# Performance work log

Hardware: AMD Instinct MI355X
Metric: run time of the kernel (lower is better)

The kernel has to match this reference:

```python
import jax, jax.numpy as jnp
import numpy as np

IN_CH = 128
OUT_CH = 32
HEADS = 4
N_NODES = 50000
N_EDGES = 500000
NEG_SLOPE = 0.01  # torch leaky_relu default


def setup_inputs() -> dict:
    key = jax.random.key(0)
    ks = jax.random.split(key, 8)
    E, D, H, C = N_EDGES, IN_CH, HEADS, OUT_CH
    receivers = jax.random.normal(ks[0], (E, D), dtype=jnp.float32)
    senders = jax.random.normal(ks[1], (E, D), dtype=jnp.float32)
    edge_attribute = jax.random.normal(ks[2], (E, D), dtype=jnp.float32)
    sender_idx = jax.random.randint(ks[3], (E,), 0, N_NODES)
    receiver_idx = jax.random.randint(ks[4], (E,), 0, N_NODES)
    # bias-free linear weights, stored as [in, heads*out] so y = x @ W
    scale = 1.0 / np.sqrt(D)
    W_src = jax.random.normal(ks[5], (D, H * C), dtype=jnp.float32) * scale
    W_tgt = jax.random.normal(ks[6], (D, H * C), dtype=jnp.float32) * scale
    W_edge = jax.random.normal(ks[7], (D, H * C), dtype=jnp.float32) * scale
    # xavier_normal_ on shape (1, H, C): std = sqrt(2/(H + C)) per torch fan calc on last two dims
    attn = jax.random.normal(jax.random.fold_in(key, 99), (1, H, C), dtype=jnp.float32) * np.sqrt(2.0 / (H + C))
    return {
        "receivers": receivers,
        "senders": senders,
        "edge_attribute": edge_attribute,
        "sender_idx": sender_idx,
        "receiver_idx": receiver_idx,
        "W_src": W_src,
        "W_tgt": W_tgt,
        "W_edge": W_edge,
        "attn": attn,
    }


def reference(receivers, senders, edge_attribute, sender_idx, receiver_idx, W_src, W_tgt, W_edge, attn):
    E = receivers.shape[0]
    H, C = HEADS, OUT_CH
    t = (receivers @ W_tgt).reshape(E, H, C)   # target projection of receiver feats
    s = (senders @ W_src).reshape(E, H, C)
    e = (edge_attribute @ W_edge).reshape(E, H, C)
    z = (jax.nn.leaky_relu(s + t + e, NEG_SLOPE) * attn).sum(-1)  # [E, H]
    # segment softmax over edges grouped by sender_idx
    zmax = jax.ops.segment_max(z, sender_idx, num_segments=N_NODES)  # [N, H]
    ez = jnp.exp(z - zmax[sender_idx])
    denom = jax.ops.segment_sum(ez, sender_idx, num_segments=N_NODES)
    a = ez / denom[sender_idx]                 # [E, H]
    m = t * a[..., None]                        # [E, H, C]
    aggr_m = jax.ops.segment_sum(m, receiver_idx, num_segments=N_NODES)  # [N, H, C]
    return aggr_m.mean(axis=1), m.mean(axis=1)  # ([N, C], [E, C])
```

## Files before the change

### kernel.cpp

```cpp
#include <hip/hip_runtime.h>
#include <hip/hip_bf16.h>

#define E_EDGES 500000
#define NN 50000

typedef unsigned short u16;
typedef __attribute__((ext_vector_type(8))) short s16x8;
typedef __attribute__((ext_vector_type(4))) float f32x4;

#define BAR() __builtin_amdgcn_s_barrier()
#define SCHED0() __builtin_amdgcn_sched_barrier(0)
#define WAITLGKM0() asm volatile("s_waitcnt lgkmcnt(0)" ::: "memory")

__device__ __forceinline__ short f2bf(float f) {
    unsigned u = __builtin_bit_cast(unsigned, f);
    u += 0x7fffu + ((u >> 16) & 1u);
    return (short)(u >> 16);
}

__device__ __forceinline__ float lrelu(float x) { return x > 0.0f ? x : 0.01f * x; }

__device__ __forceinline__ s16x8 cvt8(float4 lo, float4 hi) {
    union { s16x8 v; __hip_bfloat162 h[4]; } u;
    u.h[0] = __float22bfloat162_rn(make_float2(lo.x, lo.y));
    u.h[1] = __float22bfloat162_rn(make_float2(lo.z, lo.w));
    u.h[2] = __float22bfloat162_rn(make_float2(hi.x, hi.y));
    u.h[3] = __float22bfloat162_rn(make_float2(hi.z, hi.w));
    return u.v;
}

__global__ void kprep(const float* __restrict__ Wsrc, const float* __restrict__ Wtgt,
                      const float* __restrict__ Wedge, u16* __restrict__ WT) {
    int i = blockIdx.x * 256 + threadIdx.x;
    if (i >= 3 * 16384) return;
    int g = i >> 14, nk = i & 16383, n = nk >> 7, k = nk & 127;
    const float* W = (g == 0) ? Wsrc : (g == 1) ? Wtgt : Wedge;
    WT[i] = (u16)f2bf(W[k * 128 + n]);
}

__global__ __launch_bounds__(256, 2) void k1(
    const float* __restrict__ recv, const float* __restrict__ send,
    const float* __restrict__ eattr, const int* __restrict__ sidx,
    const u16* __restrict__ WT, const float* __restrict__ attn,
    float* __restrict__ ez, float* __restrict__ denom)
{
    __shared__ u16 ldsA[64][136];
    __shared__ u16 ldsB[128][136];
    __shared__ float smEz[64][4];
    const int tid = threadIdx.x;
    const int lane = tid & 63, wv = tid >> 6;
    const int l15 = lane & 15, lg = (lane >> 4) & 3;
    const int wm = wv >> 1, wn = wv & 1;
    const int row0 = blockIdx.x * 64;

    const float* Xg[3] = {send, eattr, recv};
    const int bgoff[3] = {0, 2 * 16384, 1 * 16384};

    f32x4 acc[2][4];
#pragma unroll
    for (int m = 0; m < 2; ++m)
#pragma unroll
        for (int ni = 0; ni < 4; ++ni) acc[m][ni] = (f32x4){0.f, 0.f, 0.f, 0.f};

    float4 ra[4][2];

    auto issueA = [&](int g) {
        const float* X = Xg[g];
#pragma unroll
        for (int q = 0; q < 4; ++q) {
            int idx = tid + 256 * q;
            int row = idx >> 4, gcol = (idx & 15) * 8;
            int ge = min(row0 + row, E_EDGES - 1);
            const float* p = X + (size_t)ge * 128 + gcol;
            ra[q][0] = *(const float4*)p;
            ra[q][1] = *(const float4*)(p + 4);
        }
    };

    auto commitA = [&]() {
#pragma unroll
        for (int q = 0; q < 4; ++q) {
            int idx = tid + 256 * q;
            *(s16x8*)&ldsA[idx >> 4][(idx & 15) * 8] = cvt8(ra[q][0], ra[q][1]);
        }
    };

    auto mfma_g = [&]() {
#pragma unroll
        for (int kk = 0; kk < 4; ++kk) {
            int k0 = kk * 32 + lg * 8;
            s16x8 a0 = *(const s16x8*)&ldsA[wm * 32 + l15][k0];
            s16x8 a1 = *(const s16x8*)&ldsA[wm * 32 + 16 + l15][k0];
#pragma unroll
            for (int ni = 0; ni < 4; ++ni) {
                s16x8 b = *(const s16x8*)&ldsB[(wn * 4 + ni) * 16 + l15][k0];
                acc[0][ni] = __builtin_amdgcn_mfma_f32_16x16x32_bf16(a0, b, acc[0][ni], 0, 0, 0);
                acc[1][ni] = __builtin_amdgcn_mfma_f32_16x16x32_bf16(a1, b, acc[1][ni], 0, 0, 0);
            }
        }
    };

    issueA(0);
#pragma unroll
    for (int g = 0; g < 3; ++g) {
        if (g) { mfma_g(); SCHED0(); }
        BAR();
        s16x8 rb[8];
        {
            const u16* Bg = WT + bgoff[g];
#pragma unroll
            for (int q = 0; q < 8; ++q) {
                int idx = tid + 256 * q;
                rb[q] = *(const s16x8*)(Bg + (idx >> 4) * 128 + (idx & 15) * 8);
            }
        }
        commitA();
        if (g < 2) issueA(g + 1);
        SCHED0();
#pragma unroll
        for (int q = 0; q < 8; ++q) {
            int idx = tid + 256 * q;
            *(s16x8*)&ldsB[idx >> 4][(idx & 15) * 8] = rb[q];
        }
        SCHED0();
        WAITLGKM0();
        BAR();
    }
    mfma_g();

    float av[4];
#pragma unroll
    for (int ni = 0; ni < 4; ++ni) av[ni] = attn[(wn * 4 + ni) * 16 + l15];

#pragma unroll
    for (int m = 0; m < 2; ++m) {
#pragma unroll
        for (int hh = 0; hh < 2; ++hh) {
            float part[4];
#pragma unroll
            for (int j = 0; j < 4; ++j)
                part[j] = lrelu(acc[m][2 * hh][j]) * av[2 * hh] +
                          lrelu(acc[m][2 * hh + 1][j]) * av[2 * hh + 1];
#pragma unroll
            for (int off = 1; off < 16; off <<= 1) {
#pragma unroll
                for (int j = 0; j < 4; ++j) part[j] += __shfl_xor(part[j], off, 64);
            }
            if (l15 == hh) {
#pragma unroll
                for (int j = 0; j < 4; ++j)
                    smEz[wm * 32 + m * 16 + lg * 4 + j][2 * wn + hh] = __expf(part[j]);
            }
        }
    }
    __syncthreads();
    {
        int row = tid >> 2, h = tid & 3;
        int r = row0 + row;
        float v = smEz[row][h];
        if (r < E_EDGES) {
            ez[(size_t)r * 4 + h] = v;
            int s = sidx[r];
            atomicAdd(&denom[(size_t)s * 4 + h], v);
        }
    }
}

__global__ __launch_bounds__(256, 2) void k2(
    const float* __restrict__ recv, const int* __restrict__ ridx,
    const int* __restrict__ sidx, const u16* __restrict__ WTt,
    const float* __restrict__ ez, const float* __restrict__ denom,
    float* __restrict__ out0, float* __restrict__ out1)
{
    __shared__ u16 ldsA[64][136];
    __shared__ u16 ldsB[128][136];
    const int tid = threadIdx.x;
    const int lane = tid & 63, wv = tid >> 6;
    const int l15 = lane & 15, lg = (lane >> 4) & 3;
    const int row0 = blockIdx.x * 64;

    float4 ra[4][2];
#pragma unroll
    for (int q = 0; q < 4; ++q) {
        int idx = tid + 256 * q;
        int row = idx >> 4, gcol = (idx & 15) * 8;
        int ge = min(row0 + row, E_EDGES - 1);
        const float* p = recv + (size_t)ge * 128 + gcol;
        ra[q][0] = *(const float4*)p;
        ra[q][1] = *(const float4*)(p + 4);
    }
    s16x8 rb[8];
#pragma unroll
    for (int q = 0; q < 8; ++q) {
        int idx = tid + 256 * q;
        rb[q] = *(const s16x8*)(WTt + (idx >> 4) * 128 + (idx & 15) * 8);
    }
#pragma unroll
    for (int q = 0; q < 4; ++q) {
        int idx = tid + 256 * q;
        *(s16x8*)&ldsA[idx >> 4][(idx & 15) * 8] = cvt8(ra[q][0], ra[q][1]);
    }
#pragma unroll
    for (int q = 0; q < 8; ++q) {
        int idx = tid + 256 * q;
        *(s16x8*)&ldsB[idx >> 4][(idx & 15) * 8] = rb[q];
    }
    __syncthreads();

    f32x4 acc[8];
#pragma unroll
    for (int n = 0; n < 8; ++n) acc[n] = (f32x4){0.f, 0.f, 0.f, 0.f};

#pragma unroll
    for (int kk = 0; kk < 4; ++kk) {
        int k0 = kk * 32 + lg * 8;
        s16x8 a = *(const s16x8*)&ldsA[wv * 16 + l15][k0];
#pragma unroll
        for (int n = 0; n < 8; ++n) {
            s16x8 b = *(const s16x8*)&ldsB[n * 16 + l15][k0];
            acc[n] = __builtin_amdgcn_mfma_f32_16x16x32_bf16(a, b, acc[n], 0, 0, 0);
        }
    }

#pragma unroll
    for (int j = 0; j < 4; ++j) {
        int r = row0 + wv * 16 + lg * 4 + j;
        if (r < E_EDGES) {
            int s = sidx[r];
            float4 ezv = *(const float4*)(ez + (size_t)r * 4);
            float4 dn = *(const float4*)(denom + (size_t)s * 4);
            float a0 = ezv.x / dn.x, a1 = ezv.y / dn.y;
            float a2 = ezv.z / dn.z, a3 = ezv.w / dn.w;
            float lo = 0.25f * (acc[0][j] * a0 + acc[2][j] * a1 +
                                acc[4][j] * a2 + acc[6][j] * a3);
            float hi = 0.25f * (acc[1][j] * a0 + acc[3][j] * a1 +
                                acc[5][j] * a2 + acc[7][j] * a3);
            out1[(size_t)r * 32 + l15] = lo;
            out1[(size_t)r * 32 + 16 + l15] = hi;
            int rv = ridx[r];
            atomicAdd(&out0[(size_t)rv * 32 + l15], lo);
            atomicAdd(&out0[(size_t)rv * 32 + 16 + l15], hi);
        }
    }
}

extern "C" void kernel_launch(void* const* d_in, const int* in_sizes, int n_in,
                              void* d_out, int out_size, void* d_ws, size_t ws_size,
                              hipStream_t stream) {
    const float* recv  = (const float*)d_in[0];
    const float* send  = (const float*)d_in[1];
    const float* eattr = (const float*)d_in[2];
    const int*   sidx  = (const int*)d_in[3];
    const int*   ridx  = (const int*)d_in[4];
    const float* Wsrc  = (const float*)d_in[5];
    const float* Wtgt  = (const float*)d_in[6];
    const float* Wedge = (const float*)d_in[7];
    const float* attn  = (const float*)d_in[8];

    char* ws = (char*)d_ws;
    u16*   WT    = (u16*)ws;
    float* ez    = (float*)(ws + 131072);
    float* denom = (float*)(ws + 131072 + 8000000);

    float* out0 = (float*)d_out;
    float* out1 = out0 + (size_t)NN * 32;

    hipMemsetAsync(denom, 0, (size_t)NN * 4 * sizeof(float), stream);
    hipMemsetAsync(out0, 0, (size_t)NN * 32 * sizeof(float), stream);

    kprep<<<192, 256, 0, stream>>>(Wsrc, Wtgt, Wedge, WT);

    int nb = (E_EDGES + 63) / 64;
    k1<<<nb, 256, 0, stream>>>(recv, send, eattr, sidx, WT, attn, ez, denom);
    k2<<<nb, 256, 0, stream>>>(recv, ridx, sidx, WT + 16384, ez, denom, out0, out1);
}
```

Measured before the change: 283.6 us.

## Make k1 persistent with register-resident weight fragments and per-wave head ownership

```diff
diff --git a/kernel.cpp b/kernel.cpp
--- a/kernel.cpp
+++ b/kernel.cpp
@@ -45,32 +45,37 @@
     float* __restrict__ ez, float* __restrict__ denom)
 {
     __shared__ u16 ldsA[64][136];
-    __shared__ u16 ldsB[128][136];
     __shared__ float smEz[64][4];
     const int tid = threadIdx.x;
     const int lane = tid & 63, wv = tid >> 6;
     const int l15 = lane & 15, lg = (lane >> 4) & 3;
-    const int wm = wv >> 1, wn = wv & 1;
-    const int row0 = blockIdx.x * 64;
+    const int b = blockIdx.x;
 
     const float* Xg[3] = {send, eattr, recv};
     const int bgoff[3] = {0, 2 * 16384, 1 * 16384};
 
-    f32x4 acc[2][4];
-#pragma unroll
-    for (int m = 0; m < 2; ++m)
-#pragma unroll
-        for (int ni = 0; ni < 4; ++ni) acc[m][ni] = (f32x4){0.f, 0.f, 0.f, 0.f};
-
+    s16x8 bfr[3][4][2];
+#pragma unroll
+    for (int g = 0; g < 3; ++g)
+#pragma unroll
+        for (int kk = 0; kk < 4; ++kk)
+#pragma unroll
+            for (int nn = 0; nn < 2; ++nn)
+                bfr[g][kk][nn] = *(const s16x8*)(WT + bgoff[g] +
+                    ((wv * 2 + nn) * 16 + l15) * 128 + kk * 32 + lg * 8);
+
+    const float av0 = attn[(wv * 2 + 0) * 16 + l15];
+    const float av1 = attn[(wv * 2 + 1) * 16 + l15];
+
+    f32x4 acc[4][2];
     float4 ra[4][2];
 
-    auto issueA = [&](int g) {
-        const float* X = Xg[g];
+    auto issueA = [&](const float* X, int tileRow) {
 #pragma unroll
         for (int q = 0; q < 4; ++q) {
             int idx = tid + 256 * q;
             int row = idx >> 4, gcol = (idx & 15) * 8;
-            int ge = min(row0 + row, E_EDGES - 1);
+            int ge = min(tileRow + row, E_EDGES - 1);
             const float* p = X + (size_t)ge * 128 + gcol;
             ra[q][0] = *(const float4*)p;
             ra[q][1] = *(const float4*)(p + 4);
@@ -85,83 +90,72 @@
         }
     };
 
-    auto mfma_g = [&]() {
+    auto mfma_ph = [&](const s16x8 (&bf)[4][2]) {
 #pragma unroll
         for (int kk = 0; kk < 4; ++kk) {
             int k0 = kk * 32 + lg * 8;
-            s16x8 a0 = *(const s16x8*)&ldsA[wm * 32 + l15][k0];
-            s16x8 a1 = *(const s16x8*)&ldsA[wm * 32 + 16 + l15][k0];
-#pragma unroll
-            for (int ni = 0; ni < 4; ++ni) {
-                s16x8 b = *(const s16x8*)&ldsB[(wn * 4 + ni) * 16 + l15][k0];
-                acc[0][ni] = __builtin_amdgcn_mfma_f32_16x16x32_bf16(a0, b, acc[0][ni], 0, 0, 0);
-                acc[1][ni] = __builtin_amdgcn_mfma_f32_16x16x32_bf16(a1, b, acc[1][ni], 0, 0, 0);
+#pragma unroll
+            for (int m = 0; m < 4; ++m) {
+                s16x8 a = *(const s16x8*)&ldsA[m * 16 + l15][k0];
+                acc[m][0] = __builtin_amdgcn_mfma_f32_16x16x32_bf16(a, bf[kk][0], acc[m][0], 0, 0, 0);
+                acc[m][1] = __builtin_amdgcn_mfma_f32_16x16x32_bf16(a, bf[kk][1], acc[m][1], 0, 0, 0);
             }
         }
     };
 
-    issueA(0);
-#pragma unroll
-    for (int g = 0; g < 3; ++g) {
-        if (g) { mfma_g(); SCHED0(); }
-        BAR();
-        s16x8 rb[8];
+    const int nt = (b < 645) ? 8 : 7;
+    issueA(Xg[0], b * 64);
+
+    for (int i = 0; i < nt; ++i) {
+        const int tile = b + i * 1024;
+        const int row0 = tile * 64;
+
+#pragma unroll
+        for (int m = 0; m < 4; ++m)
+#pragma unroll
+            for (int nn = 0; nn < 2; ++nn) acc[m][nn] = (f32x4){0.f, 0.f, 0.f, 0.f};
+
+#pragma unroll
+        for (int g = 0; g < 3; ++g) {
+            if (g == 1) { mfma_ph(bfr[0]); SCHED0(); }
+            if (g == 2) { mfma_ph(bfr[1]); SCHED0(); }
+            BAR();
+            commitA();
+            if (g < 2) issueA(Xg[g + 1], row0);
+            else if (i + 1 < nt) issueA(Xg[0], row0 + 65536);
+            SCHED0();
+            WAITLGKM0();
+            BAR();
+        }
+        mfma_ph(bfr[2]);
+
+#pragma unroll
+        for (int m = 0; m < 4; ++m) {
+            float part[4];
+#pragma unroll
+            for (int j = 0; j < 4; ++j)
+                part[j] = lrelu(acc[m][0][j]) * av0 + lrelu(acc[m][1][j]) * av1;
+#pragma unroll
+            for (int off = 1; off < 16; off <<= 1) {
+#pragma unroll
+                for (int j = 0; j < 4; ++j) part[j] += __shfl_xor(part[j], off, 64);
+            }
+            if (l15 == 0) {
+#pragma unroll
+                for (int j = 0; j < 4; ++j)
+                    smEz[m * 16 + lg * 4 + j][wv] = __expf(part[j]);
+            }
+        }
+        __syncthreads();
         {
-            const u16* Bg = WT + bgoff[g];
-#pragma unroll
-            for (int q = 0; q < 8; ++q) {
-                int idx = tid + 256 * q;
-                rb[q] = *(const s16x8*)(Bg + (idx >> 4) * 128 + (idx & 15) * 8);
-            }
-        }
-        commitA();
-        if (g < 2) issueA(g + 1);
-        SCHED0();
-#pragma unroll
-        for (int q = 0; q < 8; ++q) {
-            int idx = tid + 256 * q;
-            *(s16x8*)&ldsB[idx >> 4][(idx & 15) * 8] = rb[q];
-        }
-        SCHED0();
-        WAITLGKM0();
-        BAR();
-    }
-    mfma_g();
-
-    float av[4];
-#pragma unroll
-    for (int ni = 0; ni < 4; ++ni) av[ni] = attn[(wn * 4 + ni) * 16 + l15];
-
-#pragma unroll
-    for (int m = 0; m < 2; ++m) {
-#pragma unroll
-        for (int hh = 0; hh < 2; ++hh) {
-            float part[4];
-#pragma unroll
-            for (int j = 0; j < 4; ++j)
-                part[j] = lrelu(acc[m][2 * hh][j]) * av[2 * hh] +
-                          lrelu(acc[m][2 * hh + 1][j]) * av[2 * hh + 1];
-#pragma unroll
-            for (int off = 1; off < 16; off <<= 1) {
-#pragma unroll
-                for (int j = 0; j < 4; ++j) part[j] += __shfl_xor(part[j], off, 64);
-            }
-            if (l15 == hh) {
-#pragma unroll
-                for (int j = 0; j < 4; ++j)
-                    smEz[wm * 32 + m * 16 + lg * 4 + j][2 * wn + hh] = __expf(part[j]);
-            }
-        }
-    }
-    __syncthreads();
-    {
-        int row = tid >> 2, h = tid & 3;
-        int r = row0 + row;
-        float v = smEz[row][h];
-        if (r < E_EDGES) {
-            ez[(size_t)r * 4 + h] = v;
-            int s = sidx[r];
-            atomicAdd(&denom[(size_t)s * 4 + h], v);
+            int row = tid >> 2, h = tid & 3;
+            int r = row0 + row;
+            float v = smEz[row][h];
+            if (r < E_EDGES) {
+                ez[(size_t)r * 4 + h] = v;
+                int s = sidx[r];
+                atomicAdd(&denom[(size_t)s * 4 + h], v);
+            }
         }
     }
 }
@@ -270,7 +264,7 @@
 
     kprep<<<192, 256, 0, stream>>>(Wsrc, Wtgt, Wedge, WT);
 
-    int nb = (E_EDGES + 63) / 64;
-    k1<<<nb, 256, 0, stream>>>(recv, send, eattr, sidx, WT, attn, ez, denom);
-    k2<<<nb, 256, 0, stream>>>(recv, ridx, sidx, WT + 16384, ez, denom, out0, out1);
-}
+    k1<<<1024, 256, 0, stream>>>(recv, send, eattr, sidx, WT, attn, ez, denom);
+    int nb2 = (E_EDGES + 63) / 64;
+    k2<<<nb2, 256, 0, stream>>>(recv, ridx, sidx, WT + 16384, ez, denom, out0, out1);
+}
```

After: 276.3 us, median of 3. -2.6%, faster.
